# Performance work log

Measured on AMD Instinct MI355X. Metric: run time of the kernel, lower is better.

## Reference

```python
import jax, jax.numpy as jnp
import numpy as np

VOCAB = 32000
EMBED = 300
HIDDEN = 1150
LAYER_SIZES = [EMBED, HIDDEN, HIDDEN, EMBED]  # in->out per LSTM layer
SCALE = EMBED ** 0.5


def _lstm_layer(x, W_ih, W_hh, b_ih, b_hh):
    """Single-layer batch-first LSTM, zero initial state.
    x: [B,S,D]; W_ih: [4H,D]; W_hh: [4H,H]; biases: [4H].
    PyTorch gate order: i, f, g, o.
    Returns outputs [B,S,H]."""
    B = x.shape[0]
    H = W_hh.shape[1]
    # Precompute input contribution for all timesteps: [S,B,4H]
    x_gates = jnp.einsum('bsd,gd->sbg', x, W_ih) + (b_ih + b_hh)

    def step(carry, xg):
        h, c = carry
        gates = xg + h @ W_hh.T  # [B,4H]
        i, f, g, o = jnp.split(gates, 4, axis=-1)
        i = jax.nn.sigmoid(i)
        f = jax.nn.sigmoid(f)
        g = jnp.tanh(g)
        o = jax.nn.sigmoid(o)
        c = f * c + i * g
        h = o * jnp.tanh(c)
        return (h, c), h

    h0 = jnp.zeros((B, H), dtype=x.dtype)
    c0 = jnp.zeros((B, H), dtype=x.dtype)
    _, hs = jax.lax.scan(step, (h0, c0), x_gates)  # hs: [S,B,H]
    return hs.transpose(1, 0, 2)


def setup_inputs() -> dict:
    key = jax.random.key(0)
    ks = jax.random.split(key, 16)
    inp = {}
    inp['input_ids'] = jax.random.randint(ks[0], (16, 256), 0, VOCAB, dtype=jnp.int32)
    emb = jax.random.uniform(ks[1], (VOCAB, EMBED), dtype=jnp.float32, minval=-0.1, maxval=0.1)
    emb = emb.at[0].set(0.0)  # padding_idx = 0
    inp['embedding'] = emb
    k = 2
    for l in range(3):
        din, dout = LAYER_SIZES[l], LAYER_SIZES[l + 1]
        inp[f'W_ih{l}'] = jax.random.normal(ks[k], (4 * dout, din), dtype=jnp.float32) * (1.0 / np.sqrt(din)); k += 1
        inp[f'W_hh{l}'] = jax.random.normal(ks[k], (4 * dout, dout), dtype=jnp.float32) * (1.0 / np.sqrt(dout)); k += 1
        b_ih = jnp.zeros((4 * dout,), dtype=jnp.float32)
        b_ih = b_ih.at[dout:2 * dout].set(1.0)  # forget-gate bias = 1
        inp[f'b_ih{l}'] = b_ih
        inp[f'b_hh{l}'] = jnp.zeros((4 * dout,), dtype=jnp.float32)
    return inp


def reference(input_ids, embedding,
              W_ih0, W_hh0, b_ih0, b_hh0,
              W_ih1, W_hh1, b_ih1, b_hh1,
              W_ih2, W_hh2, b_ih2, b_hh2):
    # Eval-mode AWD-LSTM forward: all dropouts are identity; scale applied.
    x = embedding[input_ids] * SCALE  # [B,S,E]
    x = _lstm_layer(x, W_ih0, W_hh0, b_ih0, b_hh0)  # [B,S,H]
    x = _lstm_layer(x, W_ih1, W_hh1, b_ih1, b_hh1)  # [B,S,H]
    x = _lstm_layer(x, W_ih2, W_hh2, b_ih2, b_hh2)  # [B,S,E]
    # Tied output projection: Linear(E -> V, bias=False) with weight = embedding
    logits = jnp.einsum('bse,ve->bsv', x, embedding)
    return logits
```

## Files before the change

kernel.cpp:

```cpp
#include <hip/hip_runtime.h>

#define BB 16
#define SS 256
#define NVOCAB 32000
#define NEMB 300

#define CHUNK 6
#define NT 384
#define NSTR 384

typedef float f4_t __attribute__((ext_vector_type(4)));
typedef unsigned int u4_t __attribute__((ext_vector_type(4)));

__device__ __forceinline__ f4_t load_f4u(const float* p) {
    f4_t v;
    __builtin_memcpy(&v, p, sizeof(f4_t));
    return v;
}

__device__ __forceinline__ void llc_store_u4_drain(u4_t* p, u4_t v) {
    asm volatile("global_store_dwordx4 %0, %1, off sc0 sc1\n\t"
                 "s_waitcnt vmcnt(0)" :: "v"(p), "v"(v) : "memory");
}

__device__ __forceinline__ void llc_load8_wait(
        u4_t& u0, u4_t& u1, u4_t& u2, u4_t& u3,
        u4_t& u4v, u4_t& u5v, u4_t& u6v, u4_t& u7v,
        const u4_t* p0, const u4_t* p1, const u4_t* p2, const u4_t* p3,
        const u4_t* p4, const u4_t* p5, const u4_t* p6, const u4_t* p7) {
    asm volatile(
        "global_load_dwordx4 %0, %8, off sc0 sc1\n\t"
        "global_load_dwordx4 %1, %9, off sc0 sc1\n\t"
        "global_load_dwordx4 %2, %10, off sc0 sc1\n\t"
        "global_load_dwordx4 %3, %11, off sc0 sc1\n\t"
        "global_load_dwordx4 %4, %12, off sc0 sc1\n\t"
        "global_load_dwordx4 %5, %13, off sc0 sc1\n\t"
        "global_load_dwordx4 %6, %14, off sc0 sc1\n\t"
        "global_load_dwordx4 %7, %15, off sc0 sc1\n\t"
        "s_waitcnt vmcnt(0)"
        : "=&v"(u0), "=&v"(u1), "=&v"(u2), "=&v"(u3),
          "=&v"(u4v), "=&v"(u5v), "=&v"(u6v), "=&v"(u7v)
        : "v"(p0), "v"(p1), "v"(p2), "v"(p3),
          "v"(p4), "v"(p5), "v"(p6), "v"(p7)
        : "memory");
}

__global__ void embed_kernel(const int* __restrict__ ids,
                             const float* __restrict__ emb,
                             float* __restrict__ x0) {
    int bs = blockIdx.x;
    int id = ids[bs];
    const float* row = emb + (size_t)id * NEMB;
    float* out = x0 + (size_t)bs * NEMB;
    const float scale = 17.320508075688772f;
    for (int e = threadIdx.x; e < NEMB; e += blockDim.x)
        out[e] = row[e] * scale;
}

#define TM 64
#define TN 64
#define KT 16
#define LDT 68

__global__ __launch_bounds__(256) void gemm_xw(
        const float* __restrict__ A, const float* __restrict__ W,
        float* __restrict__ C, int N, int K,
        const float* __restrict__ bias_i, const float* __restrict__ bias_h,
        int permuted) {
    __shared__ __align__(16) float As[KT][LDT];
    __shared__ __align__(16) float Bs[KT][LDT];
    const int n0 = blockIdx.x * TN;
    const int m0 = blockIdx.y * TM;
    const int t  = threadIdx.x;
    const int tk = t & 15;
    const int tm = t >> 4;
    const int tx = t & 15;
    const int ty = t >> 4;
    float acc[4][4] = {};

    for (int k0 = 0; k0 < K; k0 += KT) {
        int k = k0 + tk;
        bool kok = (k < K);
        #pragma unroll
        for (int i = 0; i < 4; i++) {
            int m = tm + i * 16;
            As[tk][m] = kok ? A[(size_t)(m0 + m) * K + k] : 0.f;
            int n = n0 + m;
            Bs[tk][m] = (kok && n < N) ? W[(size_t)n * K + k] : 0.f;
        }
        __syncthreads();
        #pragma unroll
        for (int kk = 0; kk < KT; kk++) {
            float4 a = *reinterpret_cast<const float4*>(&As[kk][ty * 4]);
            float4 b = *reinterpret_cast<const float4*>(&Bs[kk][tx * 4]);
            acc[0][0] += a.x * b.x; acc[0][1] += a.x * b.y; acc[0][2] += a.x * b.z; acc[0][3] += a.x * b.w;
            acc[1][0] += a.y * b.x; acc[1][1] += a.y * b.y; acc[1][2] += a.y * b.z; acc[1][3] += a.y * b.w;
            acc[2][0] += a.z * b.x; acc[2][1] += a.z * b.y; acc[2][2] += a.z * b.z; acc[2][3] += a.z * b.w;
            acc[3][0] += a.w * b.x; acc[3][1] += a.w * b.y; acc[3][2] += a.w * b.z; acc[3][3] += a.w * b.w;
        }
        __syncthreads();
    }

    #pragma unroll
    for (int i = 0; i < 4; i++) {
        int m = m0 + ty * 4 + i;
        #pragma unroll
        for (int j = 0; j < 4; j++) {
            int n = n0 + tx * 4 + j;
            if (n < N) {
                float v = acc[i][j];
                if (bias_i) v += bias_i[n] + bias_h[n];
                size_t idx;
                if (permuted) {
                    int b_ = m >> 8;
                    int s_ = m & 255;
                    idx = ((size_t)s_ * BB + b_) * (size_t)N + n;
                } else {
                    idx = (size_t)m * (size_t)N + n;
                }
                C[idx] = v;
            }
        }
    }
}

template<int SW, int NCHR>
__global__ __launch_bounds__(NT, 1) void lstm_rec(
        const float* __restrict__ Whh,
        const float* __restrict__ xg,
        float* __restrict__ xout,
        u4_t* __restrict__ hx,
        int H, unsigned TB) {
    constexpr int KP   = 48 * SW;
    constexpr int LDH  = KP + 4;
    constexpr int NSUB = SW / 8;
    constexpr int PRS  = 17;
    constexpr int PSS  = 24 * PRS + 4;
    extern __shared__ __align__(16) float lds[];
    float* ht   = lds;
    float* pbuf = ht + 16 * LDH;
    float* gbuf = pbuf + 24 * PSS;
    float* cbuf = gbuf + NT;
    float* hlx  = cbuf + 96;

    const int t    = threadIdx.x;
    const int lane = t & 63;
    const int wv   = t >> 6;
    const int ks   = t >> 3;
    const int rg   = t & 7;
    const int h0   = blockIdx.x * CHUNK;
    const int G4   = 4 * H;

    const float* wr[3];
    #pragma unroll
    for (int j = 0; j < 3; j++) {
        int r = 3 * rg + j, g = r / CHUNK, l = r - g * CHUNK;
        int grow = ((h0 + l) < H) ? (g * H + h0 + l) : 0;
        wr[j] = Whh + (size_t)grow * (size_t)H;
    }

    for (int i = t; i < 16 * LDH; i += NT) ht[i] = 0.f;
    if (t < 96) cbuf[t] = 0.f;
    __syncthreads();

    const int r_row = t >> 4, r_b = t & 15;
    const int r_g = r_row / CHUNK, r_l = r_row - r_g * CHUNK;
    const int r_h = ((h0 + r_l) < H) ? (h0 + r_l) : h0;
    const float* xgp = xg + (size_t)r_b * G4 + (size_t)r_g * H + r_h;

    const int pairidx = (lane >> 4) & 3;
    const int prow3   = 3 * (lane & 7);

    #pragma unroll 1
    for (int s = 0; s < SS; s++) {
        const u4_t* hcb = hx + (size_t)(s & 1) * (16 * NSTR);
        u4_t*       hpb = hx + (size_t)((s + 1) & 1) * (16 * NSTR);
        const unsigned tgt = TB + (unsigned)s;
        float xgv = xgp[(size_t)s * (size_t)(16 * G4)];

        if (s > 0 && t < NCHR) {
            const u4_t* cb = hcb + t;
            #pragma unroll
            for (int rh = 0; rh < 2; rh++) {
                const u4_t* q0 = cb + (rh * 8 + 0) * NSTR;
                const u4_t* q1 = cb + (rh * 8 + 1) * NSTR;
                const u4_t* q2 = cb + (rh * 8 + 2) * NSTR;
                const u4_t* q3 = cb + (rh * 8 + 3) * NSTR;
                const u4_t* q4 = cb + (rh * 8 + 4) * NSTR;
                const u4_t* q5 = cb + (rh * 8 + 5) * NSTR;
                const u4_t* q6 = cb + (rh * 8 + 6) * NSTR;
                const u4_t* q7 = cb + (rh * 8 + 7) * NSTR;
                u4_t u0, u1, u2, u3, u4v, u5v, u6v, u7v;
                for (;;) {
                    llc_load8_wait(u0, u1, u2, u3, u4v, u5v, u6v, u7v,
                                   q0, q1, q2, q3, q4, q5, q6, q7);
                    int ok = (u0.w >= tgt) & (u1.w >= tgt) & (u2.w >= tgt) & (u3.w >= tgt)
                           & (u4v.w >= tgt) & (u5v.w >= tgt) & (u6v.w >= tgt) & (u7v.w >= tgt);
                    if (ok) break;
                }
                float* d;
                d = ht + (rh * 8 + 0) * LDH + 3 * t;
                d[0] = __uint_as_float(u0.x); d[1] = __uint_as_float(u0.y); d[2] = __uint_as_float(u0.z);
                d = ht + (rh * 8 + 1) * LDH + 3 * t;
                d[0] = __uint_as_float(u1.x); d[1] = __uint_as_float(u1.y); d[2] = __uint_as_float(u1.z);
                d = ht + (rh * 8 + 2) * LDH + 3 * t;
                d[0] = __uint_as_float(u2.x); d[1] = __uint_as_float(u2.y); d[2] = __uint_as_float(u2.z);
                d = ht + (rh * 8 + 3) * LDH + 3 * t;
                d[0] = __uint_as_float(u3.x); d[1] = __uint_as_float(u3.y); d[2] = __uint_as_float(u3.z);
                d = ht + (rh * 8 + 4) * LDH + 3 * t;
                d[0] = __uint_as_float(u4v.x); d[1] = __uint_as_float(u4v.y); d[2] = __uint_as_float(u4v.z);
                d = ht + (rh * 8 + 5) * LDH + 3 * t;
                d[0] = __uint_as_float(u5v.x); d[1] = __uint_as_float(u5v.y); d[2] = __uint_as_float(u5v.z);
                d = ht + (rh * 8 + 6) * LDH + 3 * t;
                d[0] = __uint_as_float(u6v.x); d[1] = __uint_as_float(u6v.y); d[2] = __uint_as_float(u6v.z);
                d = ht + (rh * 8 + 7) * LDH + 3 * t;
                d[0] = __uint_as_float(u7v.x); d[1] = __uint_as_float(u7v.y); d[2] = __uint_as_float(u7v.z);
            }
        }
        __syncthreads();

        float a[3][16];
        #pragma unroll
        for (int j = 0; j < 3; j++)
            #pragma unroll
            for (int b = 0; b < 16; b++) a[j][b] = 0.f;

        if (s > 0) {
            #pragma unroll
            for (int sub = 0; sub < NSUB; sub++) {
                const int kk = ks * SW + sub * 8;
                const int k0 = (kk < H) ? kk : 0;
                const int k1 = (kk + 4 < H) ? (kk + 4) : 0;
                const f4_t w00 = load_f4u(wr[0] + k0), w01 = load_f4u(wr[0] + k1);
                const f4_t w10 = load_f4u(wr[1] + k0), w11 = load_f4u(wr[1] + k1);
                const f4_t w20 = load_f4u(wr[2] + k0), w21 = load_f4u(wr[2] + k1);
                const float* hb = ht + kk;
                #pragma unroll
                for (int b = 0; b < 16; b++) {
                    const f4_t h0v = *reinterpret_cast<const f4_t*>(hb + b * LDH);
                    const f4_t h1v = *reinterpret_cast<const f4_t*>(hb + b * LDH + 4);
                    float acc;
                    acc = a[0][b];
                    acc = fmaf(w00.x, h0v.x, acc); acc = fmaf(w00.y, h0v.y, acc);
                    acc = fmaf(w00.z, h0v.z, acc); acc = fmaf(w00.w, h0v.w, acc);
                    acc = fmaf(w01.x, h1v.x, acc); acc = fmaf(w01.y, h1v.y, acc);
                    acc = fmaf(w01.z, h1v.z, acc); acc = fmaf(w01.w, h1v.w, acc);
                    a[0][b] = acc;
                    acc = a[1][b];
                    acc = fmaf(w10.x, h0v.x, acc); acc = fmaf(w10.y, h0v.y, acc);
                    acc = fmaf(w10.z, h0v.z, acc); acc = fmaf(w10.w, h0v.w, acc);
                    acc = fmaf(w11.x, h1v.x, acc); acc = fmaf(w11.y, h1v.y, acc);
                    acc = fmaf(w11.z, h1v.z, acc); acc = fmaf(w11.w, h1v.w, acc);
                    a[1][b] = acc;
                    acc = a[2][b];
                    acc = fmaf(w20.x, h0v.x, acc); acc = fmaf(w20.y, h0v.y, acc);
                    acc = fmaf(w20.z, h0v.z, acc); acc = fmaf(w20.w, h0v.w, acc);
                    acc = fmaf(w21.x, h1v.x, acc); acc = fmaf(w21.y, h1v.y, acc);
                    acc = fmaf(w21.z, h1v.z, acc); acc = fmaf(w21.w, h1v.w, acc);
                    a[2][b] = acc;
                }
            }
        }

        #pragma unroll
        for (int j = 0; j < 3; j++)
            #pragma unroll
            for (int b = 0; b < 16; b++) {
                float v = a[j][b] + __shfl_xor(a[j][b], 8);
                if ((lane & 8) == 0)
                    pbuf[(wv * 4 + pairidx) * PSS + (prow3 + j) * PRS + b] = v;
            }
        __syncthreads();

        {
            float dot = xgv;
            #pragma unroll
            for (int q = 0; q < 24; q++)
                dot += pbuf[q * PSS + r_row * PRS + r_b];
            gbuf[t] = dot;
        }
        __syncthreads();

        if (t < 96) {
            int l = t >> 4, b = t & 15;
            float gi = gbuf[(0 * CHUNK + l) * 16 + b];
            float gf = gbuf[(1 * CHUNK + l) * 16 + b];
            float gg = gbuf[(2 * CHUNK + l) * 16 + b];
            float go = gbuf[(3 * CHUNK + l) * 16 + b];
            float iv = 1.f / (1.f + expf(-gi));
            float fv = 1.f / (1.f + expf(-gf));
            float gv = tanhf(gg);
            float ov = 1.f / (1.f + expf(-go));
            float c  = fv * cbuf[t] + iv * gv;
            cbuf[t]  = c;
            float hv = ov * tanhf(c);
            hv = ((h0 + l) < H) ? hv : 0.f;
            hlx[b * CHUNK + l] = hv;
            if ((h0 + l) < H)
                xout[(size_t)b * ((size_t)SS * H) + (size_t)s * H + (h0 + l)] = hv;
        }
        __syncthreads();

        if (t < 32) {
            int bq = t >> 1, cj = t & 1;
            u4_t pk;
            pk.x = __float_as_uint(hlx[bq * CHUNK + 3 * cj + 0]);
            pk.y = __float_as_uint(hlx[bq * CHUNK + 3 * cj + 1]);
            pk.z = __float_as_uint(hlx[bq * CHUNK + 3 * cj + 2]);
            pk.w = tgt + 1u;
            llc_store_u4_drain(hpb + bq * NSTR + (h0 / 3 + cj), pk);
        }
    }
}

extern "C" void kernel_launch(void* const* d_in, const int* in_sizes, int n_in,
                              void* d_out, int out_size, void* d_ws, size_t ws_size,
                              hipStream_t stream) {
    const int*   ids  = (const int*)d_in[0];
    const float* emb  = (const float*)d_in[1];
    const float* Wih0 = (const float*)d_in[2];
    const float* Whh0 = (const float*)d_in[3];
    const float* bih0 = (const float*)d_in[4];
    const float* bhh0 = (const float*)d_in[5];
    const float* Wih1 = (const float*)d_in[6];
    const float* Whh1 = (const float*)d_in[7];
    const float* bih1 = (const float*)d_in[8];
    const float* bhh1 = (const float*)d_in[9];
    const float* Wih2 = (const float*)d_in[10];
    const float* Whh2 = (const float*)d_in[11];
    const float* bih2 = (const float*)d_in[12];
    const float* bhh2 = (const float*)d_in[13];
    float* out = (float*)d_out;

    float* ws = (float*)d_ws;
    float* xA = ws;
    float* xB = xA + 1228800;
    float* xg = xB + 4710400;
    u4_t*  hx = (u4_t*)(xg + 18841600);
    (void)in_sizes; (void)n_in; (void)out_size; (void)ws_size;

    hipMemsetAsync(hx, 0, (size_t)2 * 16 * NSTR * 16, stream);

    const size_t lds01 = (size_t)(16 * 1156 + 24 * 412 + 576) * 4;
    const size_t lds2  = (size_t)(16 * 388  + 24 * 412 + 576) * 4;

    embed_kernel<<<dim3(BB * SS), dim3(256), 0, stream>>>(ids, emb, xA);

    gemm_xw<<<dim3(72, 64), dim3(256), 0, stream>>>(xA, Wih0, xg, 4600, 300, bih0, bhh0, 1);
    lstm_rec<24, 384><<<dim3(192), dim3(NT), lds01, stream>>>(Whh0, xg, xB, hx, 1150, 0u);

    gemm_xw<<<dim3(72, 64), dim3(256), 0, stream>>>(xB, Wih1, xg, 4600, 1150, bih1, bhh1, 1);
    lstm_rec<24, 384><<<dim3(192), dim3(NT), lds01, stream>>>(Whh1, xg, xB, hx, 1150, 256u);

    gemm_xw<<<dim3(19, 64), dim3(256), 0, stream>>>(xB, Wih2, xg, 1200, 1150, bih2, bhh2, 1);
    lstm_rec<8, 100><<<dim3(50), dim3(NT), lds2, stream>>>(Whh2, xg, xA, hx, 300, 512u);

    gemm_xw<<<dim3(500, 64), dim3(256), 0, stream>>>(xA, emb, out, NVOCAB, NEMB,
                                                     nullptr, nullptr, 0);
}
```

Measured before the change: 10.35 ms.

## Use split-bf16 MFMA GEMM for vocab projection and stagger LSTM polling

Replaces the fp32 tiled GEMM for the tied output projection with a bf16 MFMA kernel. Both operands are first split into hi and lo bf16 parts, and three MFMA products recover near-fp32 accuracy. This aims to cut the large vocabulary GEMM cost, but adds two conversion passes, including a full conversion of the embedding table on every call. For layer 1 it also rotates each block's polling column and spins per-slot instead of reloading all eight, to spread contention on the shared h buffer.

```diff
diff --git a/kernel.cpp b/kernel.cpp
--- a/kernel.cpp
+++ b/kernel.cpp
@@ -11,6 +11,9 @@
 
 typedef float f4_t __attribute__((ext_vector_type(4)));
 typedef unsigned int u4_t __attribute__((ext_vector_type(4)));
+typedef short bf16x8 __attribute__((ext_vector_type(8)));
+typedef float f32x4 __attribute__((ext_vector_type(4)));
+typedef unsigned short ushort_t;
 
 __device__ __forceinline__ f4_t load_f4u(const float* p) {
     f4_t v;
@@ -45,6 +48,15 @@
         : "memory");
 }
 
+__device__ __forceinline__ u4_t llc_spin1(const u4_t* p, unsigned tgt) {
+    u4_t v;
+    do {
+        asm volatile("global_load_dwordx4 %0, %1, off sc0 sc1\n\t"
+                     "s_waitcnt vmcnt(0)" : "=v"(v) : "v"(p) : "memory");
+    } while (v.w < tgt);
+    return v;
+}
+
 __global__ void embed_kernel(const int* __restrict__ ids,
                              const float* __restrict__ emb,
                              float* __restrict__ x0) {
@@ -124,7 +136,95 @@
     }
 }
 
-template<int SW, int NCHR>
+__global__ void conv_split(const float* __restrict__ src,
+                           ushort_t* __restrict__ hi, ushort_t* __restrict__ lo,
+                           int K, int KP, int total) {
+    for (int i = blockIdx.x * blockDim.x + threadIdx.x; i < total;
+         i += gridDim.x * blockDim.x) {
+        int r = i / KP, k = i - r * KP;
+        float v = (k < K) ? src[(size_t)r * K + k] : 0.f;
+        unsigned u = __float_as_uint(v);
+        unsigned hb = (u + 0x7FFFu + ((u >> 16) & 1u)) >> 16;
+        float hf = __uint_as_float(hb << 16);
+        float rem = v - hf;
+        unsigned u2 = __float_as_uint(rem);
+        unsigned lb = (u2 + 0x7FFFu + ((u2 >> 16) & 1u)) >> 16;
+        hi[i] = (ushort_t)hb;
+        lo[i] = (ushort_t)lb;
+    }
+}
+
+__global__ __launch_bounds__(256) void gemm_mfma(
+        const ushort_t* __restrict__ Ah, const ushort_t* __restrict__ Al,
+        const ushort_t* __restrict__ Wh, const ushort_t* __restrict__ Wl,
+        float* __restrict__ C) {
+    constexpr int KP = 320, LD = 40;
+    __shared__ ushort_t sA[2][128 * LD];
+    __shared__ ushort_t sW[2][128 * LD];
+    const int t    = threadIdx.x;
+    const int lane = t & 63;
+    const int wave = t >> 6;
+    const int wm   = wave >> 1, wn = wave & 1;
+    const int n0   = blockIdx.x * 128;
+    const int m0   = blockIdx.y * 128;
+
+    f32x4 acc[4][4];
+    #pragma unroll
+    for (int i = 0; i < 4; i++)
+        #pragma unroll
+        for (int j = 0; j < 4; j++)
+            acc[i][j] = (f32x4){0.f, 0.f, 0.f, 0.f};
+
+    for (int kt = 0; kt < KP / 32; kt++) {
+        __syncthreads();
+        #pragma unroll
+        for (int c = 0; c < 2; c++) {
+            int id = t + c * 256;
+            int r = id >> 2, kq = id & 3;
+            int so = r * LD + kq * 8;
+            size_t goA = (size_t)(m0 + r) * KP + kt * 32 + kq * 8;
+            size_t goW = (size_t)(n0 + r) * KP + kt * 32 + kq * 8;
+            *reinterpret_cast<u4_t*>(&sA[0][so]) = *reinterpret_cast<const u4_t*>(Ah + goA);
+            *reinterpret_cast<u4_t*>(&sA[1][so]) = *reinterpret_cast<const u4_t*>(Al + goA);
+            *reinterpret_cast<u4_t*>(&sW[0][so]) = *reinterpret_cast<const u4_t*>(Wh + goW);
+            *reinterpret_cast<u4_t*>(&sW[1][so]) = *reinterpret_cast<const u4_t*>(Wl + goW);
+        }
+        __syncthreads();
+
+        bf16x8 ah[4], al[4], wh[4], wl[4];
+        #pragma unroll
+        for (int i = 0; i < 4; i++) {
+            int ro = (wm * 64 + i * 16 + (lane & 15)) * LD + (lane >> 4) * 8;
+            int co = (wn * 64 + i * 16 + (lane & 15)) * LD + (lane >> 4) * 8;
+            ah[i] = *reinterpret_cast<const bf16x8*>(&sA[0][ro]);
+            al[i] = *reinterpret_cast<const bf16x8*>(&sA[1][ro]);
+            wh[i] = *reinterpret_cast<const bf16x8*>(&sW[0][co]);
+            wl[i] = *reinterpret_cast<const bf16x8*>(&sW[1][co]);
+        }
+        #pragma unroll
+        for (int i = 0; i < 4; i++)
+            #pragma unroll
+            for (int j = 0; j < 4; j++) {
+                acc[i][j] = __builtin_amdgcn_mfma_f32_16x16x32_bf16(ah[i], wh[j], acc[i][j], 0, 0, 0);
+                acc[i][j] = __builtin_amdgcn_mfma_f32_16x16x32_bf16(ah[i], wl[j], acc[i][j], 0, 0, 0);
+                acc[i][j] = __builtin_amdgcn_mfma_f32_16x16x32_bf16(al[i], wh[j], acc[i][j], 0, 0, 0);
+            }
+    }
+
+    #pragma unroll
+    for (int i = 0; i < 4; i++) {
+        int row = m0 + wm * 64 + i * 16 + ((lane >> 4) << 2);
+        #pragma unroll
+        for (int j = 0; j < 4; j++) {
+            int col = n0 + wn * 64 + j * 16 + (lane & 15);
+            #pragma unroll
+            for (int r2 = 0; r2 < 4; r2++)
+                C[(size_t)(row + r2) * NVOCAB + col] = acc[i][j][r2];
+        }
+    }
+}
+
+template<int SW, int NCHR, int TGT>
 __global__ __launch_bounds__(NT, 1) void lstm_rec(
         const float* __restrict__ Whh,
         const float* __restrict__ xg,
@@ -151,6 +251,12 @@
     const int h0   = blockIdx.x * CHUNK;
     const int G4   = 4 * H;
 
+    int colT = t;
+    if constexpr (TGT) {
+        colT = t + (int)((blockIdx.x * 24u) % 384u);
+        if (colT >= 384) colT -= 384;
+    }
+
     const float* wr[3];
     #pragma unroll
     for (int j = 0; j < 3; j++) {
@@ -178,43 +284,88 @@
         const unsigned tgt = TB + (unsigned)s;
         float xgv = xgp[(size_t)s * (size_t)(16 * G4)];
 
-        if (s > 0 && t < NCHR) {
-            const u4_t* cb = hcb + t;
-            #pragma unroll
-            for (int rh = 0; rh < 2; rh++) {
-                const u4_t* q0 = cb + (rh * 8 + 0) * NSTR;
-                const u4_t* q1 = cb + (rh * 8 + 1) * NSTR;
-                const u4_t* q2 = cb + (rh * 8 + 2) * NSTR;
-                const u4_t* q3 = cb + (rh * 8 + 3) * NSTR;
-                const u4_t* q4 = cb + (rh * 8 + 4) * NSTR;
-                const u4_t* q5 = cb + (rh * 8 + 5) * NSTR;
-                const u4_t* q6 = cb + (rh * 8 + 6) * NSTR;
-                const u4_t* q7 = cb + (rh * 8 + 7) * NSTR;
-                u4_t u0, u1, u2, u3, u4v, u5v, u6v, u7v;
-                for (;;) {
+        if constexpr (TGT) {
+            if (s > 0) {
+                const u4_t* cb = hcb + colT;
+                #pragma unroll
+                for (int rh = 0; rh < 2; rh++) {
+                    const u4_t* q0 = cb + (rh * 8 + 0) * NSTR;
+                    const u4_t* q1 = cb + (rh * 8 + 1) * NSTR;
+                    const u4_t* q2 = cb + (rh * 8 + 2) * NSTR;
+                    const u4_t* q3 = cb + (rh * 8 + 3) * NSTR;
+                    const u4_t* q4 = cb + (rh * 8 + 4) * NSTR;
+                    const u4_t* q5 = cb + (rh * 8 + 5) * NSTR;
+                    const u4_t* q6 = cb + (rh * 8 + 6) * NSTR;
+                    const u4_t* q7 = cb + (rh * 8 + 7) * NSTR;
+                    u4_t u0, u1, u2, u3, u4v, u5v, u6v, u7v;
                     llc_load8_wait(u0, u1, u2, u3, u4v, u5v, u6v, u7v,
                                    q0, q1, q2, q3, q4, q5, q6, q7);
-                    int ok = (u0.w >= tgt) & (u1.w >= tgt) & (u2.w >= tgt) & (u3.w >= tgt)
-                           & (u4v.w >= tgt) & (u5v.w >= tgt) & (u6v.w >= tgt) & (u7v.w >= tgt);
-                    if (ok) break;
+                    if (u0.w  < tgt) u0  = llc_spin1(q0, tgt);
+                    if (u1.w  < tgt) u1  = llc_spin1(q1, tgt);
+                    if (u2.w  < tgt) u2  = llc_spin1(q2, tgt);
+                    if (u3.w  < tgt) u3  = llc_spin1(q3, tgt);
+                    if (u4v.w < tgt) u4v = llc_spin1(q4, tgt);
+                    if (u5v.w < tgt) u5v = llc_spin1(q5, tgt);
+                    if (u6v.w < tgt) u6v = llc_spin1(q6, tgt);
+                    if (u7v.w < tgt) u7v = llc_spin1(q7, tgt);
+                    float* d;
+                    d = ht + (rh * 8 + 0) * LDH + 3 * colT;
+                    d[0] = __uint_as_float(u0.x); d[1] = __uint_as_float(u0.y); d[2] = __uint_as_float(u0.z);
+                    d = ht + (rh * 8 + 1) * LDH + 3 * colT;
+                    d[0] = __uint_as_float(u1.x); d[1] = __uint_as_float(u1.y); d[2] = __uint_as_float(u1.z);
+                    d = ht + (rh * 8 + 2) * LDH + 3 * colT;
+                    d[0] = __uint_as_float(u2.x); d[1] = __uint_as_float(u2.y); d[2] = __uint_as_float(u2.z);
+                    d = ht + (rh * 8 + 3) * LDH + 3 * colT;
+                    d[0] = __uint_as_float(u3.x); d[1] = __uint_as_float(u3.y); d[2] = __uint_as_float(u3.z);
+                    d = ht + (rh * 8 + 4) * LDH + 3 * colT;
+                    d[0] = __uint_as_float(u4v.x); d[1] = __uint_as_float(u4v.y); d[2] = __uint_as_float(u4v.z);
+                    d = ht + (rh * 8 + 5) * LDH + 3 * colT;
+                    d[0] = __uint_as_float(u5v.x); d[1] = __uint_as_float(u5v.y); d[2] = __uint_as_float(u5v.z);
+                    d = ht + (rh * 8 + 6) * LDH + 3 * colT;
+                    d[0] = __uint_as_float(u6v.x); d[1] = __uint_as_float(u6v.y); d[2] = __uint_as_float(u6v.z);
+                    d = ht + (rh * 8 + 7) * LDH + 3 * colT;
+                    d[0] = __uint_as_float(u7v.x); d[1] = __uint_as_float(u7v.y); d[2] = __uint_as_float(u7v.z);
                 }
-                float* d;
-                d = ht + (rh * 8 + 0) * LDH + 3 * t;
-                d[0] = __uint_as_float(u0.x); d[1] = __uint_as_float(u0.y); d[2] = __uint_as_float(u0.z);
-                d = ht + (rh * 8 + 1) * LDH + 3 * t;
-                d[0] = __uint_as_float(u1.x); d[1] = __uint_as_float(u1.y); d[2] = __uint_as_float(u1.z);
-                d = ht + (rh * 8 + 2) * LDH + 3 * t;
-                d[0] = __uint_as_float(u2.x); d[1] = __uint_as_float(u2.y); d[2] = __uint_as_float(u2.z);
-                d = ht + (rh * 8 + 3) * LDH + 3 * t;
-                d[0] = __uint_as_float(u3.x); d[1] = __uint_as_float(u3.y); d[2] = __uint_as_float(u3.z);
-                d = ht + (rh * 8 + 4) * LDH + 3 * t;
-                d[0] = __uint_as_float(u4v.x); d[1] = __uint_as_float(u4v.y); d[2] = __uint_as_float(u4v.z);
-                d = ht + (rh * 8 + 5) * LDH + 3 * t;
-                d[0] = __uint_as_float(u5v.x); d[1] = __uint_as_float(u5v.y); d[2] = __uint_as_float(u5v.z);
-                d = ht + (rh * 8 + 6) * LDH + 3 * t;
-                d[0] = __uint_as_float(u6v.x); d[1] = __uint_as_float(u6v.y); d[2] = __uint_as_float(u6v.z);
-                d = ht + (rh * 8 + 7) * LDH + 3 * t;
-                d[0] = __uint_as_float(u7v.x); d[1] = __uint_as_float(u7v.y); d[2] = __uint_as_float(u7v.z);
+            }
+        } else {
+            if (s > 0 && t < NCHR) {
+                const u4_t* cb = hcb + t;
+                #pragma unroll
+                for (int rh = 0; rh < 2; rh++) {
+                    const u4_t* q0 = cb + (rh * 8 + 0) * NSTR;
+                    const u4_t* q1 = cb + (rh * 8 + 1) * NSTR;
+                    const u4_t* q2 = cb + (rh * 8 + 2) * NSTR;
+                    const u4_t* q3 = cb + (rh * 8 + 3) * NSTR;
+                    const u4_t* q4 = cb + (rh * 8 + 4) * NSTR;
+                    const u4_t* q5 = cb + (rh * 8 + 5) * NSTR;
+                    const u4_t* q6 = cb + (rh * 8 + 6) * NSTR;
+                    const u4_t* q7 = cb + (rh * 8 + 7) * NSTR;
+                    u4_t u0, u1, u2, u3, u4v, u5v, u6v, u7v;
+                    for (;;) {
+                        llc_load8_wait(u0, u1, u2, u3, u4v, u5v, u6v, u7v,
+                                       q0, q1, q2, q3, q4, q5, q6, q7);
+                        int ok = (u0.w >= tgt) & (u1.w >= tgt) & (u2.w >= tgt) & (u3.w >= tgt)
+                               & (u4v.w >= tgt) & (u5v.w >= tgt) & (u6v.w >= tgt) & (u7v.w >= tgt);
+                        if (ok) break;
+                    }
+                    float* d;
+                    d = ht + (rh * 8 + 0) * LDH + 3 * t;
+                    d[0] = __uint_as_float(u0.x); d[1] = __uint_as_float(u0.y); d[2] = __uint_as_float(u0.z);
+                    d = ht + (rh * 8 + 1) * LDH + 3 * t;
+                    d[0] = __uint_as_float(u1.x); d[1] = __uint_as_float(u1.y); d[2] = __uint_as_float(u1.z);
+                    d = ht + (rh * 8 + 2) * LDH + 3 * t;
+                    d[0] = __uint_as_float(u2.x); d[1] = __uint_as_float(u2.y); d[2] = __uint_as_float(u2.z);
+                    d = ht + (rh * 8 + 3) * LDH + 3 * t;
+                    d[0] = __uint_as_float(u3.x); d[1] = __uint_as_float(u3.y); d[2] = __uint_as_float(u3.z);
+                    d = ht + (rh * 8 + 4) * LDH + 3 * t;
+                    d[0] = __uint_as_float(u4v.x); d[1] = __uint_as_float(u4v.y); d[2] = __uint_as_float(u4v.z);
+                    d = ht + (rh * 8 + 5) * LDH + 3 * t;
+                    d[0] = __uint_as_float(u5v.x); d[1] = __uint_as_float(u5v.y); d[2] = __uint_as_float(u5v.z);
+                    d = ht + (rh * 8 + 6) * LDH + 3 * t;
+                    d[0] = __uint_as_float(u6v.x); d[1] = __uint_as_float(u6v.y); d[2] = __uint_as_float(u6v.z);
+                    d = ht + (rh * 8 + 7) * LDH + 3 * t;
+                    d[0] = __uint_as_float(u7v.x); d[1] = __uint_as_float(u7v.y); d[2] = __uint_as_float(u7v.z);
+                }
             }
         }
         __syncthreads();
@@ -339,6 +490,11 @@
     u4_t*  hx = (u4_t*)(xg + 18841600);
     (void)in_sizes; (void)n_in; (void)out_size; (void)ws_size;
 
+    ushort_t* Ah = (ushort_t*)xB;
+    ushort_t* Al = Ah + (size_t)4096 * 320;
+    ushort_t* Wh = (ushort_t*)xg;
+    ushort_t* Wl = Wh + (size_t)32000 * 320;
+
     hipMemsetAsync(hx, 0, (size_t)2 * 16 * NSTR * 16, stream);
 
     const size_t lds01 = (size_t)(16 * 1156 + 24 * 412 + 576) * 4;
@@ -347,14 +503,16 @@
     embed_kernel<<<dim3(BB * SS), dim3(256), 0, stream>>>(ids, emb, xA);
 
     gemm_xw<<<dim3(72, 64), dim3(256), 0, stream>>>(xA, Wih0, xg, 4600, 300, bih0, bhh0, 1);
-    lstm_rec<24, 384><<<dim3(192), dim3(NT), lds01, stream>>>(Whh0, xg, xB, hx, 1150, 0u);
+    lstm_rec<24, 384, 0><<<dim3(192), dim3(NT), lds01, stream>>>(Whh0, xg, xB, hx, 1150, 0u);
 
     gemm_xw<<<dim3(72, 64), dim3(256), 0, stream>>>(xB, Wih1, xg, 4600, 1150, bih1, bhh1, 1);
-    lstm_rec<24, 384><<<dim3(192), dim3(NT), lds01, stream>>>(Whh1, xg, xB, hx, 1150, 256u);
+    lstm_rec<24, 384, 1><<<dim3(192), dim3(NT), lds01, stream>>>(Whh1, xg, xB, hx, 1150, 256u);
 
     gemm_xw<<<dim3(19, 64), dim3(256), 0, stream>>>(xB, Wih2, xg, 1200, 1150, bih2, bhh2, 1);
-    lstm_rec<8, 100><<<dim3(50), dim3(NT), lds2, stream>>>(Whh2, xg, xA, hx, 300, 512u);
-
-    gemm_xw<<<dim3(500, 64), dim3(256), 0, stream>>>(xA, emb, out, NVOCAB, NEMB,
-                                                     nullptr, nullptr, 0);
-}
+    lstm_rec<8, 100, 0><<<dim3(50), dim3(NT), lds2, stream>>>(Whh2, xg, xA, hx, 300, 512u);
+
+    conv_split<<<dim3(640), dim3(256), 0, stream>>>(xA, Ah, Al, 300, 320, 4096 * 320);
+    conv_split<<<dim3(2048), dim3(256), 0, stream>>>(emb, Wh, Wl, 300, 320, 32000 * 320);
+
+    gemm_mfma<<<dim3(250, 32), dim3(256), 0, stream>>>(Ah, Al, Wh, Wl, out);
+}
```

After: 10.13 ms. 1.02x faster.

## Replace FP32 SIMT GEMMs with split-bf16 MFMA GEMMs and restructure LSTM h exchange

Applied to the files above, without the earlier changes.

The input-projection and output-logit GEMMs move from a scalar FP32 tiled kernel to MFMA bf16 matrix instructions. Each FP32 operand is split into hi+lo bf16 parts and three products are accumulated to keep near-FP32 accuracy. Conversion kernels run before each GEMM and use the output buffer and workspace as scratch. The recurrent kernel also changes the hidden-state exchange layout so each polling thread reads 16 contiguous vectors with one base pointer, and it fuses the gate nonlinearity with the packed store to drop one barrier. The risks are the added conversion passes, extra memory traffic, and a small loss of precision.

```diff
diff --git a/kernel.cpp b/kernel.cpp
--- a/kernel.cpp
+++ b/kernel.cpp
@@ -11,6 +11,9 @@
 
 typedef float f4_t __attribute__((ext_vector_type(4)));
 typedef unsigned int u4_t __attribute__((ext_vector_type(4)));
+typedef short bf16x8 __attribute__((ext_vector_type(8)));
+typedef float f32x4 __attribute__((ext_vector_type(4)));
+typedef unsigned short ushort_t;
 
 __device__ __forceinline__ f4_t load_f4u(const float* p) {
     f4_t v;
@@ -23,25 +26,35 @@
                  "s_waitcnt vmcnt(0)" :: "v"(p), "v"(v) : "memory");
 }
 
-__device__ __forceinline__ void llc_load8_wait(
-        u4_t& u0, u4_t& u1, u4_t& u2, u4_t& u3,
-        u4_t& u4v, u4_t& u5v, u4_t& u6v, u4_t& u7v,
-        const u4_t* p0, const u4_t* p1, const u4_t* p2, const u4_t* p3,
-        const u4_t* p4, const u4_t* p5, const u4_t* p6, const u4_t* p7) {
+__device__ __forceinline__ void llc_load16_wait(
+        u4_t& a0, u4_t& a1, u4_t& a2, u4_t& a3,
+        u4_t& a4, u4_t& a5, u4_t& a6, u4_t& a7,
+        u4_t& a8, u4_t& a9, u4_t& a10, u4_t& a11,
+        u4_t& a12, u4_t& a13, u4_t& a14, u4_t& a15,
+        const u4_t* p) {
     asm volatile(
-        "global_load_dwordx4 %0, %8, off sc0 sc1\n\t"
-        "global_load_dwordx4 %1, %9, off sc0 sc1\n\t"
-        "global_load_dwordx4 %2, %10, off sc0 sc1\n\t"
-        "global_load_dwordx4 %3, %11, off sc0 sc1\n\t"
-        "global_load_dwordx4 %4, %12, off sc0 sc1\n\t"
-        "global_load_dwordx4 %5, %13, off sc0 sc1\n\t"
-        "global_load_dwordx4 %6, %14, off sc0 sc1\n\t"
-        "global_load_dwordx4 %7, %15, off sc0 sc1\n\t"
+        "global_load_dwordx4 %0, %16, off sc0 sc1\n\t"
+        "global_load_dwordx4 %1, %16, off offset:256 sc0 sc1\n\t"
+        "global_load_dwordx4 %2, %16, off offset:512 sc0 sc1\n\t"
+        "global_load_dwordx4 %3, %16, off offset:768 sc0 sc1\n\t"
+        "global_load_dwordx4 %4, %16, off offset:1024 sc0 sc1\n\t"
+        "global_load_dwordx4 %5, %16, off offset:1280 sc0 sc1\n\t"
+        "global_load_dwordx4 %6, %16, off offset:1536 sc0 sc1\n\t"
+        "global_load_dwordx4 %7, %16, off offset:1792 sc0 sc1\n\t"
+        "global_load_dwordx4 %8, %16, off offset:2048 sc0 sc1\n\t"
+        "global_load_dwordx4 %9, %16, off offset:2304 sc0 sc1\n\t"
+        "global_load_dwordx4 %10, %16, off offset:2560 sc0 sc1\n\t"
+        "global_load_dwordx4 %11, %16, off offset:2816 sc0 sc1\n\t"
+        "global_load_dwordx4 %12, %16, off offset:3072 sc0 sc1\n\t"
+        "global_load_dwordx4 %13, %16, off offset:3328 sc0 sc1\n\t"
+        "global_load_dwordx4 %14, %16, off offset:3584 sc0 sc1\n\t"
+        "global_load_dwordx4 %15, %16, off offset:3840 sc0 sc1\n\t"
         "s_waitcnt vmcnt(0)"
-        : "=&v"(u0), "=&v"(u1), "=&v"(u2), "=&v"(u3),
-          "=&v"(u4v), "=&v"(u5v), "=&v"(u6v), "=&v"(u7v)
-        : "v"(p0), "v"(p1), "v"(p2), "v"(p3),
-          "v"(p4), "v"(p5), "v"(p6), "v"(p7)
+        : "=&v"(a0), "=&v"(a1), "=&v"(a2), "=&v"(a3),
+          "=&v"(a4), "=&v"(a5), "=&v"(a6), "=&v"(a7),
+          "=&v"(a8), "=&v"(a9), "=&v"(a10), "=&v"(a11),
+          "=&v"(a12), "=&v"(a13), "=&v"(a14), "=&v"(a15)
+        : "v"(p)
         : "memory");
 }
 
@@ -57,68 +70,106 @@
         out[e] = row[e] * scale;
 }
 
-#define TM 64
-#define TN 64
-#define KT 16
-#define LDT 68
-
-__global__ __launch_bounds__(256) void gemm_xw(
-        const float* __restrict__ A, const float* __restrict__ W,
-        float* __restrict__ C, int N, int K,
+__global__ void conv_split(const float* __restrict__ src,
+                           ushort_t* __restrict__ hi, ushort_t* __restrict__ lo,
+                           int N, int K, int KP, int total) {
+    for (int i = blockIdx.x * blockDim.x + threadIdx.x; i < total;
+         i += gridDim.x * blockDim.x) {
+        int r = i / KP, k = i - r * KP;
+        float v = (r < N && k < K) ? src[(size_t)r * K + k] : 0.f;
+        unsigned u = __float_as_uint(v);
+        unsigned hb = (u + 0x7FFFu + ((u >> 16) & 1u)) >> 16;
+        float hf = __uint_as_float(hb << 16);
+        float rem = v - hf;
+        unsigned u2 = __float_as_uint(rem);
+        unsigned lb = (u2 + 0x7FFFu + ((u2 >> 16) & 1u)) >> 16;
+        hi[i] = (ushort_t)hb;
+        lo[i] = (ushort_t)lb;
+    }
+}
+
+__global__ __launch_bounds__(256) void gemm_mfma(
+        const ushort_t* __restrict__ Ah, const ushort_t* __restrict__ Al,
+        const ushort_t* __restrict__ Wh, const ushort_t* __restrict__ Wl,
+        float* __restrict__ C, int N, int KP,
         const float* __restrict__ bias_i, const float* __restrict__ bias_h,
         int permuted) {
-    __shared__ __align__(16) float As[KT][LDT];
-    __shared__ __align__(16) float Bs[KT][LDT];
-    const int n0 = blockIdx.x * TN;
-    const int m0 = blockIdx.y * TM;
-    const int t  = threadIdx.x;
-    const int tk = t & 15;
-    const int tm = t >> 4;
-    const int tx = t & 15;
-    const int ty = t >> 4;
-    float acc[4][4] = {};
-
-    for (int k0 = 0; k0 < K; k0 += KT) {
-        int k = k0 + tk;
-        bool kok = (k < K);
+    constexpr int LD = 40;
+    __shared__ ushort_t sA[2][128 * LD];
+    __shared__ ushort_t sW[2][128 * LD];
+    const int t    = threadIdx.x;
+    const int lane = t & 63;
+    const int wave = t >> 6;
+    const int wm   = wave >> 1, wn = wave & 1;
+    const int n0   = blockIdx.x * 128;
+    const int m0   = blockIdx.y * 128;
+
+    f32x4 acc[4][4];
+    #pragma unroll
+    for (int i = 0; i < 4; i++)
+        #pragma unroll
+        for (int j = 0; j < 4; j++)
+            acc[i][j] = (f32x4){0.f, 0.f, 0.f, 0.f};
+
+    const int nkt = KP >> 5;
+    for (int kt = 0; kt < nkt; kt++) {
+        __syncthreads();
+        #pragma unroll
+        for (int c = 0; c < 2; c++) {
+            int id = t + c * 256;
+            int r = id >> 2, kq = id & 3;
+            int so = r * LD + kq * 8;
+            size_t goA = (size_t)(m0 + r) * KP + kt * 32 + kq * 8;
+            size_t goW = (size_t)(n0 + r) * KP + kt * 32 + kq * 8;
+            *reinterpret_cast<u4_t*>(&sA[0][so]) = *reinterpret_cast<const u4_t*>(Ah + goA);
+            *reinterpret_cast<u4_t*>(&sA[1][so]) = *reinterpret_cast<const u4_t*>(Al + goA);
+            *reinterpret_cast<u4_t*>(&sW[0][so]) = *reinterpret_cast<const u4_t*>(Wh + goW);
+            *reinterpret_cast<u4_t*>(&sW[1][so]) = *reinterpret_cast<const u4_t*>(Wl + goW);
+        }
+        __syncthreads();
+
+        bf16x8 ah[4], al[4], wh[4], wl[4];
         #pragma unroll
         for (int i = 0; i < 4; i++) {
-            int m = tm + i * 16;
-            As[tk][m] = kok ? A[(size_t)(m0 + m) * K + k] : 0.f;
-            int n = n0 + m;
-            Bs[tk][m] = (kok && n < N) ? W[(size_t)n * K + k] : 0.f;
-        }
-        __syncthreads();
-        #pragma unroll
-        for (int kk = 0; kk < KT; kk++) {
-            float4 a = *reinterpret_cast<const float4*>(&As[kk][ty * 4]);
-            float4 b = *reinterpret_cast<const float4*>(&Bs[kk][tx * 4]);
-            acc[0][0] += a.x * b.x; acc[0][1] += a.x * b.y; acc[0][2] += a.x * b.z; acc[0][3] += a.x * b.w;
-            acc[1][0] += a.y * b.x; acc[1][1] += a.y * b.y; acc[1][2] += a.y * b.z; acc[1][3] += a.y * b.w;
-            acc[2][0] += a.z * b.x; acc[2][1] += a.z * b.y; acc[2][2] += a.z * b.z; acc[2][3] += a.z * b.w;
-            acc[3][0] += a.w * b.x; acc[3][1] += a.w * b.y; acc[3][2] += a.w * b.z; acc[3][3] += a.w * b.w;
-        }
-        __syncthreads();
+            int ro = (wm * 64 + i * 16 + (lane & 15)) * LD + (lane >> 4) * 8;
+            int co = (wn * 64 + i * 16 + (lane & 15)) * LD + (lane >> 4) * 8;
+            ah[i] = *reinterpret_cast<const bf16x8*>(&sA[0][ro]);
+            al[i] = *reinterpret_cast<const bf16x8*>(&sA[1][ro]);
+            wh[i] = *reinterpret_cast<const bf16x8*>(&sW[0][co]);
+            wl[i] = *reinterpret_cast<const bf16x8*>(&sW[1][co]);
+        }
+        #pragma unroll
+        for (int i = 0; i < 4; i++)
+            #pragma unroll
+            for (int j = 0; j < 4; j++) {
+                acc[i][j] = __builtin_amdgcn_mfma_f32_16x16x32_bf16(ah[i], wh[j], acc[i][j], 0, 0, 0);
+                acc[i][j] = __builtin_amdgcn_mfma_f32_16x16x32_bf16(ah[i], wl[j], acc[i][j], 0, 0, 0);
+                acc[i][j] = __builtin_amdgcn_mfma_f32_16x16x32_bf16(al[i], wh[j], acc[i][j], 0, 0, 0);
+            }
     }
 
     #pragma unroll
     for (int i = 0; i < 4; i++) {
-        int m = m0 + ty * 4 + i;
+        int row = m0 + wm * 64 + i * 16 + ((lane >> 4) << 2);
         #pragma unroll
         for (int j = 0; j < 4; j++) {
-            int n = n0 + tx * 4 + j;
-            if (n < N) {
-                float v = acc[i][j];
-                if (bias_i) v += bias_i[n] + bias_h[n];
-                size_t idx;
-                if (permuted) {
-                    int b_ = m >> 8;
-                    int s_ = m & 255;
-                    idx = ((size_t)s_ * BB + b_) * (size_t)N + n;
-                } else {
-                    idx = (size_t)m * (size_t)N + n;
+            int col = n0 + wn * 64 + j * 16 + (lane & 15);
+            if (col < N) {
+                float bv = bias_i ? (bias_i[col] + bias_h[col]) : 0.f;
+                #pragma unroll
+                for (int r2 = 0; r2 < 4; r2++) {
+                    int m = row + r2;
+                    float v = acc[i][j][r2] + bv;
+                    size_t idx;
+                    if (permuted) {
+                        int b_ = m >> 8;
+                        int s_ = m & 255;
+                        idx = ((size_t)s_ * BB + b_) * (size_t)N + col;
+                    } else {
+                        idx = (size_t)m * (size_t)N + col;
+                    }
+                    C[idx] = v;
                 }
-                C[idx] = v;
             }
         }
     }
@@ -141,7 +192,6 @@
     float* pbuf = ht + 16 * LDH;
     float* gbuf = pbuf + 24 * PSS;
     float* cbuf = gbuf + NT;
-    float* hlx  = cbuf + 96;
 
     const int t    = threadIdx.x;
     const int lane = t & 63;
@@ -171,6 +221,8 @@
     const int pairidx = (lane >> 4) & 3;
     const int prow3   = 3 * (lane & 7);
 
+    const int stg_base = (t >> 4) * 256 + (t & 15);
+
     #pragma unroll 1
     for (int s = 0; s < SS; s++) {
         const u4_t* hcb = hx + (size_t)(s & 1) * (16 * NSTR);
@@ -179,43 +231,35 @@
         float xgv = xgp[(size_t)s * (size_t)(16 * G4)];
 
         if (s > 0 && t < NCHR) {
-            const u4_t* cb = hcb + t;
-            #pragma unroll
-            for (int rh = 0; rh < 2; rh++) {
-                const u4_t* q0 = cb + (rh * 8 + 0) * NSTR;
-                const u4_t* q1 = cb + (rh * 8 + 1) * NSTR;
-                const u4_t* q2 = cb + (rh * 8 + 2) * NSTR;
-                const u4_t* q3 = cb + (rh * 8 + 3) * NSTR;
-                const u4_t* q4 = cb + (rh * 8 + 4) * NSTR;
-                const u4_t* q5 = cb + (rh * 8 + 5) * NSTR;
-                const u4_t* q6 = cb + (rh * 8 + 6) * NSTR;
-                const u4_t* q7 = cb + (rh * 8 + 7) * NSTR;
-                u4_t u0, u1, u2, u3, u4v, u5v, u6v, u7v;
-                for (;;) {
-                    llc_load8_wait(u0, u1, u2, u3, u4v, u5v, u6v, u7v,
-                                   q0, q1, q2, q3, q4, q5, q6, q7);
-                    int ok = (u0.w >= tgt) & (u1.w >= tgt) & (u2.w >= tgt) & (u3.w >= tgt)
-                           & (u4v.w >= tgt) & (u5v.w >= tgt) & (u6v.w >= tgt) & (u7v.w >= tgt);
-                    if (ok) break;
-                }
-                float* d;
-                d = ht + (rh * 8 + 0) * LDH + 3 * t;
-                d[0] = __uint_as_float(u0.x); d[1] = __uint_as_float(u0.y); d[2] = __uint_as_float(u0.z);
-                d = ht + (rh * 8 + 1) * LDH + 3 * t;
-                d[0] = __uint_as_float(u1.x); d[1] = __uint_as_float(u1.y); d[2] = __uint_as_float(u1.z);
-                d = ht + (rh * 8 + 2) * LDH + 3 * t;
-                d[0] = __uint_as_float(u2.x); d[1] = __uint_as_float(u2.y); d[2] = __uint_as_float(u2.z);
-                d = ht + (rh * 8 + 3) * LDH + 3 * t;
-                d[0] = __uint_as_float(u3.x); d[1] = __uint_as_float(u3.y); d[2] = __uint_as_float(u3.z);
-                d = ht + (rh * 8 + 4) * LDH + 3 * t;
-                d[0] = __uint_as_float(u4v.x); d[1] = __uint_as_float(u4v.y); d[2] = __uint_as_float(u4v.z);
-                d = ht + (rh * 8 + 5) * LDH + 3 * t;
-                d[0] = __uint_as_float(u5v.x); d[1] = __uint_as_float(u5v.y); d[2] = __uint_as_float(u5v.z);
-                d = ht + (rh * 8 + 6) * LDH + 3 * t;
-                d[0] = __uint_as_float(u6v.x); d[1] = __uint_as_float(u6v.y); d[2] = __uint_as_float(u6v.z);
-                d = ht + (rh * 8 + 7) * LDH + 3 * t;
-                d[0] = __uint_as_float(u7v.x); d[1] = __uint_as_float(u7v.y); d[2] = __uint_as_float(u7v.z);
-            }
+            const u4_t* p = hcb + stg_base;
+            u4_t u0, u1, u2, u3, u4v, u5v, u6v, u7v;
+            u4_t u8v, u9v, u10v, u11v, u12v, u13v, u14v, u15v;
+            for (;;) {
+                llc_load16_wait(u0, u1, u2, u3, u4v, u5v, u6v, u7v,
+                                u8v, u9v, u10v, u11v, u12v, u13v, u14v, u15v, p);
+                int ok = (u0.w  >= tgt) & (u1.w  >= tgt) & (u2.w  >= tgt) & (u3.w  >= tgt)
+                       & (u4v.w >= tgt) & (u5v.w >= tgt) & (u6v.w >= tgt) & (u7v.w >= tgt)
+                       & (u8v.w >= tgt) & (u9v.w >= tgt) & (u10v.w >= tgt) & (u11v.w >= tgt)
+                       & (u12v.w >= tgt) & (u13v.w >= tgt) & (u14v.w >= tgt) & (u15v.w >= tgt);
+                if (ok) break;
+            }
+            float* d;
+            d = ht +  0 * LDH + 3 * t; d[0] = __uint_as_float(u0.x);  d[1] = __uint_as_float(u0.y);  d[2] = __uint_as_float(u0.z);
+            d = ht +  1 * LDH + 3 * t; d[0] = __uint_as_float(u1.x);  d[1] = __uint_as_float(u1.y);  d[2] = __uint_as_float(u1.z);
+            d = ht +  2 * LDH + 3 * t; d[0] = __uint_as_float(u2.x);  d[1] = __uint_as_float(u2.y);  d[2] = __uint_as_float(u2.z);
+            d = ht +  3 * LDH + 3 * t; d[0] = __uint_as_float(u3.x);  d[1] = __uint_as_float(u3.y);  d[2] = __uint_as_float(u3.z);
+            d = ht +  4 * LDH + 3 * t; d[0] = __uint_as_float(u4v.x); d[1] = __uint_as_float(u4v.y); d[2] = __uint_as_float(u4v.z);
+            d = ht +  5 * LDH + 3 * t; d[0] = __uint_as_float(u5v.x); d[1] = __uint_as_float(u5v.y); d[2] = __uint_as_float(u5v.z);
+            d = ht +  6 * LDH + 3 * t; d[0] = __uint_as_float(u6v.x); d[1] = __uint_as_float(u6v.y); d[2] = __uint_as_float(u6v.z);
+            d = ht +  7 * LDH + 3 * t; d[0] = __uint_as_float(u7v.x); d[1] = __uint_as_float(u7v.y); d[2] = __uint_as_float(u7v.z);
+            d = ht +  8 * LDH + 3 * t; d[0] = __uint_as_float(u8v.x); d[1] = __uint_as_float(u8v.y); d[2] = __uint_as_float(u8v.z);
+            d = ht +  9 * LDH + 3 * t; d[0] = __uint_as_float(u9v.x); d[1] = __uint_as_float(u9v.y); d[2] = __uint_as_float(u9v.z);
+            d = ht + 10 * LDH + 3 * t; d[0] = __uint_as_float(u10v.x); d[1] = __uint_as_float(u10v.y); d[2] = __uint_as_float(u10v.z);
+            d = ht + 11 * LDH + 3 * t; d[0] = __uint_as_float(u11v.x); d[1] = __uint_as_float(u11v.y); d[2] = __uint_as_float(u11v.z);
+            d = ht + 12 * LDH + 3 * t; d[0] = __uint_as_float(u12v.x); d[1] = __uint_as_float(u12v.y); d[2] = __uint_as_float(u12v.z);
+            d = ht + 13 * LDH + 3 * t; d[0] = __uint_as_float(u13v.x); d[1] = __uint_as_float(u13v.y); d[2] = __uint_as_float(u13v.z);
+            d = ht + 14 * LDH + 3 * t; d[0] = __uint_as_float(u14v.x); d[1] = __uint_as_float(u14v.y); d[2] = __uint_as_float(u14v.z);
+            d = ht + 15 * LDH + 3 * t; d[0] = __uint_as_float(u15v.x); d[1] = __uint_as_float(u15v.y); d[2] = __uint_as_float(u15v.z);
         }
         __syncthreads();
 
@@ -281,34 +325,37 @@
         }
         __syncthreads();
 
-        if (t < 96) {
-            int l = t >> 4, b = t & 15;
-            float gi = gbuf[(0 * CHUNK + l) * 16 + b];
-            float gf = gbuf[(1 * CHUNK + l) * 16 + b];
-            float gg = gbuf[(2 * CHUNK + l) * 16 + b];
-            float go = gbuf[(3 * CHUNK + l) * 16 + b];
-            float iv = 1.f / (1.f + expf(-gi));
-            float fv = 1.f / (1.f + expf(-gf));
-            float gv = tanhf(gg);
-            float ov = 1.f / (1.f + expf(-go));
-            float c  = fv * cbuf[t] + iv * gv;
-            cbuf[t]  = c;
-            float hv = ov * tanhf(c);
-            hv = ((h0 + l) < H) ? hv : 0.f;
-            hlx[b * CHUNK + l] = hv;
-            if ((h0 + l) < H)
-                xout[(size_t)b * ((size_t)SS * H) + (size_t)s * H + (h0 + l)] = hv;
-        }
-        __syncthreads();
-
         if (t < 32) {
-            int bq = t >> 1, cj = t & 1;
+            const int b = t & 15, cj = t >> 4;
+            float hv3[3];
+            #pragma unroll
+            for (int i = 0; i < 3; i++) {
+                int l = 3 * cj + i;
+                float gi = gbuf[(0 * CHUNK + l) * 16 + b];
+                float gf = gbuf[(1 * CHUNK + l) * 16 + b];
+                float gg = gbuf[(2 * CHUNK + l) * 16 + b];
+                float go = gbuf[(3 * CHUNK + l) * 16 + b];
+                float iv = 1.f / (1.f + expf(-gi));
+                float fv = 1.f / (1.f + expf(-gf));
+                float gv = tanhf(gg);
+                float ov = 1.f / (1.f + expf(-go));
+                int ci = l * 16 + b;
+                float c = fv * cbuf[ci] + iv * gv;
+                cbuf[ci] = c;
+                float hv = ov * tanhf(c);
+                int hidx = h0 + l;
+                if (hidx >= H) hv = 0.f;
+                hv3[i] = hv;
+                if (hidx < H)
+                    xout[(size_t)b * ((size_t)SS * H) + (size_t)s * H + hidx] = hv;
+            }
             u4_t pk;
-            pk.x = __float_as_uint(hlx[bq * CHUNK + 3 * cj + 0]);
-            pk.y = __float_as_uint(hlx[bq * CHUNK + 3 * cj + 1]);
-            pk.z = __float_as_uint(hlx[bq * CHUNK + 3 * cj + 2]);
+            pk.x = __float_as_uint(hv3[0]);
+            pk.y = __float_as_uint(hv3[1]);
+            pk.z = __float_as_uint(hv3[2]);
             pk.w = tgt + 1u;
-            llc_store_u4_drain(hpb + bq * NSTR + (h0 / 3 + cj), pk);
+            int c = (h0 / 3) + cj;
+            llc_store_u4_drain(hpb + ((c >> 4) * 256 + b * 16 + (c & 15)), pk);
         }
     }
 }
@@ -339,22 +386,50 @@
     u4_t*  hx = (u4_t*)(xg + 18841600);
     (void)in_sizes; (void)n_in; (void)out_size; (void)ws_size;
 
+    ushort_t* sc  = (ushort_t*)d_out;
+    ushort_t* tAh = sc;
+    ushort_t* tAl = tAh + (size_t)4096 * 1152;
+    ushort_t* W0h = tAl + (size_t)4096 * 1152;
+    ushort_t* W0l = W0h + (size_t)4608 * 320;
+    ushort_t* W1h = W0l + (size_t)4608 * 320;
+    ushort_t* W1l = W1h + (size_t)4608 * 1152;
+    ushort_t* W2h = W1l + (size_t)4608 * 1152;
+    ushort_t* W2l = W2h + (size_t)1280 * 1152;
+
+    ushort_t* fAh = (ushort_t*)xB;
+    ushort_t* fAl = fAh + (size_t)4096 * 320;
+    ushort_t* fWh = (ushort_t*)xg;
+    ushort_t* fWl = fWh + (size_t)32000 * 320;
+
     hipMemsetAsync(hx, 0, (size_t)2 * 16 * NSTR * 16, stream);
 
-    const size_t lds01 = (size_t)(16 * 1156 + 24 * 412 + 576) * 4;
-    const size_t lds2  = (size_t)(16 * 388  + 24 * 412 + 576) * 4;
+    const size_t lds01 = (size_t)(16 * 1156 + 24 * 412 + NT + 96) * 4;
+    const size_t lds2  = (size_t)(16 * 388  + 24 * 412 + NT + 96) * 4;
+
+    conv_split<<<dim3(720), dim3(256), 0, stream>>>(Wih0, W0h, W0l, 4600, 300, 320, 4608 * 320);
+    conv_split<<<dim3(2048), dim3(256), 0, stream>>>(Wih1, W1h, W1l, 4600, 1150, 1152, 4608 * 1152);
+    conv_split<<<dim3(720), dim3(256), 0, stream>>>(Wih2, W2h, W2l, 1200, 1150, 1152, 1280 * 1152);
 
     embed_kernel<<<dim3(BB * SS), dim3(256), 0, stream>>>(ids, emb, xA);
 
-    gemm_xw<<<dim3(72, 64), dim3(256), 0, stream>>>(xA, Wih0, xg, 4600, 300, bih0, bhh0, 1);
+    conv_split<<<dim3(640), dim3(256), 0, stream>>>(xA, tAh, tAl, 4096, 300, 320, 4096 * 320);
+    gemm_mfma<<<dim3(36, 32), dim3(256), 0, stream>>>(tAh, tAl, W0h, W0l, xg,
+                                                      4600, 320, bih0, bhh0, 1);
     lstm_rec<24, 384><<<dim3(192), dim3(NT), lds01, stream>>>(Whh0, xg, xB, hx, 1150, 0u);
 
-    gemm_xw<<<dim3(72, 64), dim3(256), 0, stream>>>(xB, Wih1, xg, 4600, 1150, bih1, bhh1, 1);
+    conv_split<<<dim3(2048), dim3(256), 0, stream>>>(xB, tAh, tAl, 4096, 1150, 1152, 4096 * 1152);
+    gemm_mfma<<<dim3(36, 32), dim3(256), 0, stream>>>(tAh, tAl, W1h, W1l, xg,
+                                                      4600, 1152, bih1, bhh1, 1);
     lstm_rec<24, 384><<<dim3(192), dim3(NT), lds01, stream>>>(Whh1, xg, xB, hx, 1150, 256u);
 
-    gemm_xw<<<dim3(19, 64), dim3(256), 0, stream>>>(xB, Wih2, xg, 1200, 1150, bih2, bhh2, 1);
+    conv_split<<<dim3(2048), dim3(256), 0, stream>>>(xB, tAh, tAl, 4096, 1150, 1152, 4096 * 1152);
+    gemm_mfma<<<dim3(10, 32), dim3(256), 0, stream>>>(tAh, tAl, W2h, W2l, xg,
+                                                      1200, 1152, bih2, bhh2, 1);
     lstm_rec<8, 100><<<dim3(50), dim3(NT), lds2, stream>>>(Whh2, xg, xA, hx, 300, 512u);
 
-    gemm_xw<<<dim3(500, 64), dim3(256), 0, stream>>>(xA, emb, out, NVOCAB, NEMB,
-                                                     nullptr, nullptr, 0);
-}
+    conv_split<<<dim3(640), dim3(256), 0, stream>>>(xA, fAh, fAl, 4096, 300, 320, 4096 * 320);
+    conv_split<<<dim3(2048), dim3(256), 0, stream>>>(emb, fWh, fWl, 32000, 300, 320, 32000 * 320);
+
+    gemm_mfma<<<dim3(250, 32), dim3(256), 0, stream>>>(fAh, fAl, fWh, fWl, out,
+                                                       NVOCAB, 320, nullptr, nullptr, 0);
+}
```

Measured after the change: 10.91 ms. 1.05x slower.
